# Kernel optimization log

Hardware: AMD Instinct MI355X
Metric: run time of the kernel (lower is better)

## Reference

```python
import jax, jax.numpy as jnp
import numpy as np

N = 50000
E = 800000
NFEAT = 128
NHID = 128
NCLASS = 40
NUM_HOPS = 4


def setup_inputs() -> dict:
    key = jax.random.key(0)
    ks = jax.random.split(key, 8)
    stdv = 1.0 / np.sqrt(NHID)
    features = jax.random.normal(ks[0], (N, NFEAT), dtype=jnp.float32)
    edge_row = jax.random.randint(ks[1], (E,), 0, N, dtype=jnp.int32)
    edge_col = jax.random.randint(ks[2], (E,), 0, N, dtype=jnp.int32)
    edge_val = jax.random.uniform(ks[3], (E,), dtype=jnp.float32) / 16.0  # ~normalized adj
    Wg = jax.random.uniform(ks[4], (NUM_HOPS, NHID, NHID), minval=-stdv, maxval=stdv, dtype=jnp.float32)
    att_w = jax.random.uniform(ks[5], (NFEAT + NHID,), minval=-stdv, maxval=stdv, dtype=jnp.float32)
    att_b = jnp.zeros((1,), dtype=jnp.float32)
    fc_w = jax.random.uniform(ks[6], (NHID, NCLASS), minval=-stdv, maxval=stdv, dtype=jnp.float32)
    fc_b = jnp.zeros((NCLASS,), dtype=jnp.float32)
    return {"features": features, "edge_row": edge_row, "edge_col": edge_col,
            "edge_val": edge_val, "Wg": Wg, "att_w": att_w, "att_b": att_b,
            "fc_w": fc_w, "fc_b": fc_b}


def _spmm(edge_row, edge_col, edge_val, x):
    # sparse (COO) adj @ x : gather source rows, scale, scatter-add to dest rows
    return jax.ops.segment_sum(edge_val[:, None] * x[edge_col], edge_row, num_segments=N)


def reference(features, edge_row, edge_col, edge_val, Wg, att_w, att_b, fc_w, fc_b):
    h_list = [features]
    h = features
    for i in range(NUM_HOPS):
        h = _spmm(edge_row, edge_col, edge_val, h)
        h = jax.nn.relu(h @ Wg[i])  # dropout is identity in eval mode
        h_list.append(h)

    # attention: sigmoid(Linear(cat(h_k, h0))) for each hop output h_k
    H = jnp.stack(h_list[1:], axis=0)          # [K, N, nhid]
    w_h, w_f = att_w[:NHID], att_w[NHID:]      # cat order is (x, features)
    scores = jax.nn.sigmoid(jnp.einsum('knh,h->kn', H, w_h)
                            + (features @ w_f)[None, :] + att_b[0])  # [K, N]
    W = jax.nn.softmax(scores, axis=0)         # softmax over hops, per node

    # faithful to original loop: h_list[1]*W0 + sum_{i=1..K-1} h_list[i]*W_i
    output = h_list[1] * W[0][:, None]
    for i in range(1, NUM_HOPS):
        output = output + h_list[i] * W[i][:, None]

    logits = output @ fc_w + fc_b
    return jax.nn.log_softmax(logits, axis=1)
```

## Files before the change

### kernel.cpp

```cpp
#include <hip/hip_runtime.h>
#include <cmath>

#define N      50000
#define E      800000
#define NFEAT  128
#define NHID   128
#define NCLASS 40
#define NUM_HOPS 4
#define NF     (N * NHID)
#define NBKT   196
#define BCAP   5888
#define XSTR   132
#define HSTR   136
#define HROWS  16
#define SC1_EPT 16
#define SC1_BLK ((E + 256 * SC1_EPT - 1) / (256 * SC1_EPT))

typedef __attribute__((ext_vector_type(8))) short bf16x8;
typedef __attribute__((ext_vector_type(4))) float f32x4;

__device__ __forceinline__ unsigned bf16pack(float a, float b) {
    unsigned ua = __float_as_uint(a), ub = __float_as_uint(b);
    ua = (ua + 0x7fffu + ((ua >> 16) & 1u)) >> 16;
    ub = (ub + 0x7fffu + ((ub >> 16) & 1u)) >> 16;
    return ua | (ub << 16);
}
__device__ __forceinline__ unsigned short bf16s(float x) {
    unsigned u = __float_as_uint(x);
    u = (u + 0x7fffu + ((u >> 16) & 1u)) >> 16;
    return (unsigned short)u;
}
__device__ __forceinline__ float bf16lo(unsigned u) { return __uint_as_float(u << 16); }
__device__ __forceinline__ float bf16hi(unsigned u) { return __uint_as_float(u & 0xffff0000u); }


__global__ void k_binit2(int* __restrict__ bcur) {
    int b = threadIdx.x;
    if (b < NBKT) bcur[b] = b * BCAP;
}

__global__ __launch_bounds__(256) void k_scat1(const int* __restrict__ row,
                                               const int* __restrict__ col,
                                               const float* __restrict__ val,
                                               int* __restrict__ bcur,
                                               unsigned long long* __restrict__ evt) {
    __shared__ int lhist[NBKT];
    __shared__ int gbase[NBKT];
    __shared__ int lcur[NBKT];
    int t = threadIdx.x;
    int e0 = blockIdx.x * (256 * SC1_EPT);
    for (int i = t; i < NBKT; i += 256) { lhist[i] = 0; lcur[i] = 0; }
    __syncthreads();
    int rows[SC1_EPT];
#pragma unroll
    for (int i = 0; i < SC1_EPT; ++i) {
        int e = e0 + i * 256 + t;
        int r = (e < E) ? row[e] : -1;
        rows[i] = r;
        if (r >= 0) atomicAdd(&lhist[r >> 8], 1);
    }
    __syncthreads();
    for (int i = t; i < NBKT; i += 256) {
        int c = lhist[i];
        gbase[i] = c ? atomicAdd(&bcur[i], c) : 0;
    }
    __syncthreads();
#pragma unroll
    for (int i = 0; i < SC1_EPT; ++i) {
        int r = rows[i];
        if (r >= 0) {
            int e = e0 + i * 256 + t;
            int b = r >> 8;
            int off = atomicAdd(&lcur[b], 1);
            size_t idx = (size_t)gbase[b] + off;
            if (idx < (size_t)(b + 1) * BCAP) {
                unsigned v = __float_as_uint(val[e]);
                v = (v + 0x7fffu + ((v >> 16) & 1u)) & 0xffff0000u;
                evt[idx] = ((unsigned long long)(r & 255) << 32)
                         | ((unsigned)col[e] | v);
            }
        }
    }
}

__global__ __launch_bounds__(256) void k_scat2b(const int* __restrict__ bcur,
                                                const unsigned long long* __restrict__ evt,
                                                unsigned* __restrict__ ev,
                                                int* __restrict__ rpb,
                                                int* __restrict__ rpe) {
    __shared__ int lhist[256];
    __shared__ int ws[4];
    __shared__ int cur[256];
    int b = blockIdx.x;
    int t = threadIdx.x;
    int base = b * BCAP;
    int ecnt = bcur[b] - base;
    if (ecnt > BCAP) ecnt = BCAP;
    lhist[t] = 0;
    __syncthreads();
    for (int i = t; i < ecnt; i += 256)
        atomicAdd(&lhist[(int)(evt[(size_t)base + i] >> 32)], 1);
    __syncthreads();
    int cntr = lhist[t];
    int pc = (cntr + 3) & ~3;
    int lane = t & 63, wv_ = t >> 6;
    int incl = pc;
    for (int off = 1; off < 64; off <<= 1) {
        int u = __shfl_up(incl, off);
        if (lane >= off) incl += u;
    }
    if (lane == 63) ws[wv_] = incl;
    __syncthreads();
    int woff = 0;
    for (int k = 0; k < wv_; ++k) woff += ws[k];
    int rowbeg = base + (incl - pc + woff);
    int rt = b * 256 + t;
    if (rt < N) { rpb[rt] = rowbeg; rpe[rt] = rowbeg + pc; }
    cur[t] = rowbeg;
    __syncthreads();
    for (int i = t; i < ecnt; i += 256) {
        unsigned long long e = evt[(size_t)base + i];
        int r8 = (int)(e >> 32);
        int p = atomicAdd(&cur[r8], 1);
        ev[p] = (unsigned)e;
    }
    __syncthreads();
    int e1 = rowbeg + pc;
    for (int p = cur[t]; p < e1; ++p) ev[p] = 0;
}


__global__ void k_cvtf(const float* __restrict__ f, const float* __restrict__ att_w,
                       float* __restrict__ fs, unsigned short* __restrict__ fb) {
    int node = (blockIdx.x * blockDim.x + threadIdx.x) >> 6;
    if (node >= N) return;
    int lane = threadIdx.x & 63;
    const float2 wf = ((const float2*)(att_w + NHID))[lane];
    const float2 fv = ((const float2*)(f + (size_t)node * NFEAT))[lane];
    ((unsigned*)(fb + (size_t)node * NFEAT))[lane] = bf16pack(fv.x, fv.y);
    float s = fv.x * wf.x + fv.y * wf.y;
    for (int off = 32; off; off >>= 1) s += __shfl_xor(s, off);
    if (lane == 0) fs[node] = s;
}

__global__ void k_cvt_w(const float* __restrict__ Wg, unsigned short* __restrict__ Wbt) {
    int idx = blockIdx.x * blockDim.x + threadIdx.x;
    if (idx >= NUM_HOPS * NHID * NHID) return;
    int i = idx >> 14;
    int rem = idx & 16383;
    int n = rem >> 7;
    int k = rem & 127;
    Wbt[idx] = bf16s(Wg[(i << 14) + k * NHID + n]);
}


__global__ __launch_bounds__(256) void k_hop(const int* __restrict__ rpb,
                                             const int* __restrict__ rpe,
                                             const unsigned* __restrict__ ev,
                                             const unsigned short* __restrict__ xb,
                                             const unsigned short* __restrict__ Wbt,
                                             const float* __restrict__ att_w,
                                             unsigned short* __restrict__ yb,
                                             float* __restrict__ Sh) {
    __shared__ unsigned short xsm[HROWS * HSTR];
    __shared__ float sS[HROWS][4];
    int t = threadIdx.x;
    int w = t >> 6;
    int lane = t & 63;
    int quad = lane >> 4;
    int l15 = lane & 15;
    int rowb = blockIdx.x * HROWS;
    const uint4* xq = (const uint4*)xb;

#define ACC8(g, v)                                                            \
    do {                                                                      \
        a0 = fmaf((v), bf16lo((g).x), a0); a1 = fmaf((v), bf16hi((g).x), a1); \
        a2 = fmaf((v), bf16lo((g).y), a2); a3 = fmaf((v), bf16hi((g).y), a3); \
        a4 = fmaf((v), bf16lo((g).z), a4); a5 = fmaf((v), bf16hi((g).z), a5); \
        a6 = fmaf((v), bf16lo((g).w), a6); a7 = fmaf((v), bf16hi((g).w), a7); \
    } while (0)
    {
        int rl  = t >> 4;
        int row = rowb + rl;
        float a0 = 0.f, a1 = 0.f, a2 = 0.f, a3 = 0.f;
        float a4 = 0.f, a5 = 0.f, a6 = 0.f, a7 = 0.f;
        if (row < N) {
            int beg = rpb[row], end = rpe[row];
            int j = beg;
            for (; j + 8 <= end; j += 8) {
                uint4 p0 = *(const uint4*)(ev + j);
                uint4 p1 = *(const uint4*)(ev + j + 4);
                uint4 g0 = xq[(size_t)(p0.x & 0xffffu) * 16 + l15];
                uint4 g1 = xq[(size_t)(p0.y & 0xffffu) * 16 + l15];
                uint4 g2 = xq[(size_t)(p0.z & 0xffffu) * 16 + l15];
                uint4 g3 = xq[(size_t)(p0.w & 0xffffu) * 16 + l15];
                uint4 g4 = xq[(size_t)(p1.x & 0xffffu) * 16 + l15];
                uint4 g5 = xq[(size_t)(p1.y & 0xffffu) * 16 + l15];
                uint4 g6 = xq[(size_t)(p1.z & 0xffffu) * 16 + l15];
                uint4 g7 = xq[(size_t)(p1.w & 0xffffu) * 16 + l15];
                ACC8(g0, bf16hi(p0.x));
                ACC8(g1, bf16hi(p0.y));
                ACC8(g2, bf16hi(p0.z));
                ACC8(g3, bf16hi(p0.w));
                ACC8(g4, bf16hi(p1.x));
                ACC8(g5, bf16hi(p1.y));
                ACC8(g6, bf16hi(p1.z));
                ACC8(g7, bf16hi(p1.w));
            }
            if (j < end) {
                uint4 p0 = *(const uint4*)(ev + j);
                uint4 g0 = xq[(size_t)(p0.x & 0xffffu) * 16 + l15];
                uint4 g1 = xq[(size_t)(p0.y & 0xffffu) * 16 + l15];
                uint4 g2 = xq[(size_t)(p0.z & 0xffffu) * 16 + l15];
                uint4 g3 = xq[(size_t)(p0.w & 0xffffu) * 16 + l15];
                ACC8(g0, bf16hi(p0.x));
                ACC8(g1, bf16hi(p0.y));
                ACC8(g2, bf16hi(p0.z));
                ACC8(g3, bf16hi(p0.w));
            }
        }
        uint4 o;
        o.x = bf16pack(a0, a1);
        o.y = bf16pack(a2, a3);
        o.z = bf16pack(a4, a5);
        o.w = bf16pack(a6, a7);
        *(uint4*)(xsm + (size_t)rl * HSTR + l15 * 8) = o;
    }
#undef ACC8
    __syncthreads();

    bf16x8 af[4];
#pragma unroll
    for (int s = 0; s < 4; ++s) {
        uint4 ua = *(const uint4*)(xsm + (size_t)l15 * HSTR + s * 32 + quad * 8);
        af[s] = __builtin_bit_cast(bf16x8, ua);
    }

    f32x4 acc[2];
#pragma unroll
    for (int nt = 0; nt < 2; ++nt) acc[nt] = (f32x4){0.f, 0.f, 0.f, 0.f};

#pragma unroll
    for (int nt = 0; nt < 2; ++nt) {
        int ntg = w * 2 + nt;
#pragma unroll
        for (int s = 0; s < 4; ++s) {
            uint4 ub = *(const uint4*)(Wbt + ((size_t)(ntg * 16 + l15) * NHID + s * 32 + quad * 8));
            bf16x8 bfv = __builtin_bit_cast(bf16x8, ub);
            acc[nt] = __builtin_amdgcn_mfma_f32_16x16x32_bf16(af[s], bfv, acc[nt], 0, 0, 0);
        }
    }

    float whl[2];
#pragma unroll
    for (int nt = 0; nt < 2; ++nt) whl[nt] = att_w[(w * 2 + nt) * 16 + l15];

    float scr[4] = {0.f, 0.f, 0.f, 0.f};
#pragma unroll
    for (int nt = 0; nt < 2; ++nt) {
#pragma unroll
        for (int r = 0; r < 4; ++r) {
            float v = fmaxf(acc[nt][r], 0.f);
            scr[r] = fmaf(v, whl[nt], scr[r]);
            int grow = rowb + quad * 4 + r;
            if (grow < N)
                yb[(size_t)grow * NHID + (w * 2 + nt) * 16 + l15] = bf16s(v);
        }
    }
#pragma unroll
    for (int r = 0; r < 4; ++r) {
        float p = scr[r];
        p += __shfl_xor(p, 1);
        p += __shfl_xor(p, 2);
        p += __shfl_xor(p, 4);
        p += __shfl_xor(p, 8);
        if (l15 == 0) sS[quad * 4 + r][w] = p;
    }
    __syncthreads();
    if (t < HROWS) {
        int grow = rowb + t;
        if (grow < N) Sh[grow] = sS[t][0] + sS[t][1] + sS[t][2] + sS[t][3];
    }
}


__global__ __launch_bounds__(256) void k_attn_final(const unsigned short* __restrict__ hb,
                                                    const float* __restrict__ S,
                                                    const float* __restrict__ fs,
                                                    const float* __restrict__ att_b,
                                                    const float* __restrict__ fc_w,
                                                    const float* __restrict__ fc_b,
                                                    float* __restrict__ out) {
    __shared__ float xs[64 * XSTR];
    __shared__ float wv[4][64];
    int t = threadIdx.x;
    int base = blockIdx.x * 64;

    if (t < 64) {
        int node = base + t;
        if (node < N) {
            float b = att_b[0] + fs[node];
            float g0 = 1.f / (1.f + __expf(-(S[0 * N + node] + b)));
            float g1 = 1.f / (1.f + __expf(-(S[1 * N + node] + b)));
            float g2 = 1.f / (1.f + __expf(-(S[2 * N + node] + b)));
            float g3 = 1.f / (1.f + __expf(-(S[3 * N + node] + b)));
            float m = fmaxf(fmaxf(g0, g1), fmaxf(g2, g3));
            float e0 = __expf(g0 - m), e1 = __expf(g1 - m);
            float e2 = __expf(g2 - m), e3 = __expf(g3 - m);
            float inv = 1.f / (e0 + e1 + e2 + e3);
            wv[0][t] = e0 * inv; wv[1][t] = e1 * inv;
            wv[2][t] = e2 * inv; wv[3][t] = e3 * inv;
        } else {
            wv[0][t] = 0.f; wv[1][t] = 0.f; wv[2][t] = 0.f; wv[3][t] = 0.f;
        }
    }
    __syncthreads();

#pragma unroll
    for (int qq = 0; qq < 4; ++qq) {
        int idx = qq * 256 + t;
        int nl = idx >> 4;
        int d8 = idx & 15;
        int node = base + nl;
        float o[8] = {0.f, 0.f, 0.f, 0.f, 0.f, 0.f, 0.f, 0.f};
        if (node < N) {
            float w0 = wv[0][nl], w1 = wv[1][nl], w2 = wv[2][nl], w3 = wv[3][nl];
            uint4 u0 = ((const uint4*)(hb + 0 * (size_t)NF + (size_t)node * NHID))[d8];
            uint4 u1 = ((const uint4*)(hb + 1 * (size_t)NF + (size_t)node * NHID))[d8];
            uint4 u2 = ((const uint4*)(hb + 2 * (size_t)NF + (size_t)node * NHID))[d8];
            uint4 u3 = ((const uint4*)(hb + 3 * (size_t)NF + (size_t)node * NHID))[d8];
            o[0] = w0 * bf16lo(u0.x) + w1 * bf16lo(u1.x) + w2 * bf16lo(u2.x) + w3 * bf16lo(u3.x);
            o[1] = w0 * bf16hi(u0.x) + w1 * bf16hi(u1.x) + w2 * bf16hi(u2.x) + w3 * bf16hi(u3.x);
            o[2] = w0 * bf16lo(u0.y) + w1 * bf16lo(u1.y) + w2 * bf16lo(u2.y) + w3 * bf16lo(u3.y);
            o[3] = w0 * bf16hi(u0.y) + w1 * bf16hi(u1.y) + w2 * bf16hi(u2.y) + w3 * bf16hi(u3.y);
            o[4] = w0 * bf16lo(u0.z) + w1 * bf16lo(u1.z) + w2 * bf16lo(u2.z) + w3 * bf16lo(u3.z);
            o[5] = w0 * bf16hi(u0.z) + w1 * bf16hi(u1.z) + w2 * bf16hi(u2.z) + w3 * bf16hi(u3.z);
            o[6] = w0 * bf16lo(u0.w) + w1 * bf16lo(u1.w) + w2 * bf16lo(u2.w) + w3 * bf16lo(u3.w);
            o[7] = w0 * bf16hi(u0.w) + w1 * bf16hi(u1.w) + w2 * bf16hi(u2.w) + w3 * bf16hi(u3.w);
        }
        float* xp = &xs[nl * XSTR + (d8 << 3)];
        *(float4*)xp       = make_float4(o[0], o[1], o[2], o[3]);
        *(float4*)(xp + 4) = make_float4(o[4], o[5], o[6], o[7]);
    }
    __syncthreads();

    int cq = t & 15;
    int rg = t >> 4;
    int cb = (cq < 10) ? (cq << 2) : 36;
    float4 bias = *(const float4*)(fc_b + cb);
    float4 acc[4];
#pragma unroll
    for (int r = 0; r < 4; ++r) acc[r] = bias;
    for (int k4 = 0; k4 < NHID / 4; ++k4) {
        float4 w0 = *(const float4*)(fc_w + (size_t)(4 * k4 + 0) * NCLASS + cb);
        float4 w1 = *(const float4*)(fc_w + (size_t)(4 * k4 + 1) * NCLASS + cb);
        float4 w2 = *(const float4*)(fc_w + (size_t)(4 * k4 + 2) * NCLASS + cb);
        float4 w3 = *(const float4*)(fc_w + (size_t)(4 * k4 + 3) * NCLASS + cb);
#pragma unroll
        for (int r = 0; r < 4; ++r) {
            float4 xv = *(const float4*)&xs[(rg * 4 + r) * XSTR + (k4 << 2)];
            acc[r].x = fmaf(xv.x, w0.x, acc[r].x);
            acc[r].y = fmaf(xv.x, w0.y, acc[r].y);
            acc[r].z = fmaf(xv.x, w0.z, acc[r].z);
            acc[r].w = fmaf(xv.x, w0.w, acc[r].w);
            acc[r].x = fmaf(xv.y, w1.x, acc[r].x);
            acc[r].y = fmaf(xv.y, w1.y, acc[r].y);
            acc[r].z = fmaf(xv.y, w1.z, acc[r].z);
            acc[r].w = fmaf(xv.y, w1.w, acc[r].w);
            acc[r].x = fmaf(xv.z, w2.x, acc[r].x);
            acc[r].y = fmaf(xv.z, w2.y, acc[r].y);
            acc[r].z = fmaf(xv.z, w2.z, acc[r].z);
            acc[r].w = fmaf(xv.z, w2.w, acc[r].w);
            acc[r].x = fmaf(xv.w, w3.x, acc[r].x);
            acc[r].y = fmaf(xv.w, w3.y, acc[r].y);
            acc[r].z = fmaf(xv.w, w3.z, acc[r].z);
            acc[r].w = fmaf(xv.w, w3.w, acc[r].w);
        }
    }
#pragma unroll
    for (int r = 0; r < 4; ++r) {
        int nd = base + rg * 4 + r;
        float mloc = (cq < 10)
            ? fmaxf(fmaxf(acc[r].x, acc[r].y), fmaxf(acc[r].z, acc[r].w))
            : -INFINITY;
        float m = mloc;
        m = fmaxf(m, __shfl_xor(m, 1));
        m = fmaxf(m, __shfl_xor(m, 2));
        m = fmaxf(m, __shfl_xor(m, 4));
        m = fmaxf(m, __shfl_xor(m, 8));
        float sloc = (cq < 10)
            ? (__expf(acc[r].x - m) + __expf(acc[r].y - m) +
               __expf(acc[r].z - m) + __expf(acc[r].w - m))
            : 0.f;
        float s = sloc;
        s += __shfl_xor(s, 1);
        s += __shfl_xor(s, 2);
        s += __shfl_xor(s, 4);
        s += __shfl_xor(s, 8);
        float ls = m + logf(s);
        if (cq < 10 && nd < N) {
            float4 o;
            o.x = acc[r].x - ls;
            o.y = acc[r].y - ls;
            o.z = acc[r].z - ls;
            o.w = acc[r].w - ls;
            *(float4*)(out + (size_t)nd * NCLASS + cb) = o;
        }
    }
}


extern "C" void kernel_launch(void* const* d_in, const int* in_sizes, int n_in,
                              void* d_out, int out_size, void* d_ws, size_t ws_size,
                              hipStream_t stream) {
    const float* features = (const float*)d_in[0];
    const int*   erow     = (const int*)d_in[1];
    const int*   ecol     = (const int*)d_in[2];
    const float* eval_    = (const float*)d_in[3];
    const float* Wg       = (const float*)d_in[4];
    const float* att_w    = (const float*)d_in[5];
    const float* att_b    = (const float*)d_in[6];
    const float* fc_w     = (const float*)d_in[7];
    const float* fc_b     = (const float*)d_in[8];
    float*       out      = (float*)d_out;

    const size_t SLOTS = 2 * (size_t)NF
                       + (size_t)NF / 2
                       + 32768
                       + (size_t)NBKT * BCAP
                       + 3 * (size_t)N
                       + NBKT
                       + 4 * (size_t)N;
    if (ws_size < SLOTS * 4) return;

    unsigned short* hbb  = (unsigned short*)d_ws;
    unsigned short* fb   = hbb + 4 * (size_t)NF;
    unsigned short* Wbt  = fb + (size_t)NF;
    unsigned*       ev   = (unsigned*)(Wbt + 65536);
    int*            rpb  = (int*)(ev + (size_t)NBKT * BCAP);
    int*            rpe  = rpb + N;
    float*          fs   = (float*)(rpe + N);
    int*            bcur = (int*)(fs + N);
    float*          S    = (float*)(bcur + NBKT);
    unsigned long long* evt = (unsigned long long*)hbb;

    k_binit2<<<1, 256, 0, stream>>>(bcur);
    k_scat1<<<SC1_BLK, 256, 0, stream>>>(erow, ecol, eval_, bcur, evt);
    k_scat2b<<<NBKT, 256, 0, stream>>>(bcur, evt, ev, rpb, rpe);

    k_cvtf<<<(N * 64 + 255) / 256, 256, 0, stream>>>(features, att_w, fs, fb);
    k_cvt_w<<<(NUM_HOPS * NHID * NHID + 255) / 256, 256, 0, stream>>>(Wg, Wbt);

    const unsigned short* xb = fb;
    for (int i = 0; i < NUM_HOPS; ++i) {
        k_hop<<<(N + HROWS - 1) / HROWS, 256, 0, stream>>>(rpb, rpe, ev, xb,
                                                 Wbt + (size_t)i * NHID * NHID,
                                                 att_w, hbb + (size_t)i * NF,
                                                 S + (size_t)i * N);
        xb = hbb + (size_t)i * NF;
    }

    k_attn_final<<<(N + 63) / 64, 256, 0, stream>>>(hbb, S, fs, att_b, fc_w, fc_b, out);
}
```

Before: 308.5 us.

## Sort rows by degree so hop blocks process similar-length rows together

Adds a counting sort of nodes by padded row length (histogram, scan, scatter) that builds a permutation, then has each hop kernel process rows in permuted order and write outputs back to the original row positions. The goal is to cut load imbalance and wave divergence when rows of very different degree share a block. In exchange it adds three small kernels, an extra indirection per row, and scattered output stores that are less coalesced.

```diff
diff --git a/kernel.cpp b/kernel.cpp
--- a/kernel.cpp
+++ b/kernel.cpp
@@ -13,6 +13,7 @@
 #define XSTR   132
 #define HSTR   136
 #define HROWS  16
+#define DBINS  1024
 #define SC1_EPT 16
 #define SC1_BLK ((E + 256 * SC1_EPT - 1) / (256 * SC1_EPT))
 
@@ -34,9 +35,10 @@
 __device__ __forceinline__ float bf16hi(unsigned u) { return __uint_as_float(u & 0xffff0000u); }
 
 
-__global__ void k_binit2(int* __restrict__ bcur) {
-    int b = threadIdx.x;
-    if (b < NBKT) bcur[b] = b * BCAP;
+__global__ void k_binit2(int* __restrict__ bcur, int* __restrict__ dhist) {
+    int t = threadIdx.x;
+    if (t < NBKT) bcur[t] = t * BCAP;
+    for (int i = t; i < DBINS; i += 256) dhist[i] = 0;
 }
 
 __global__ __launch_bounds__(256) void k_scat1(const int* __restrict__ row,
@@ -130,6 +132,51 @@
 }
 
 
+__global__ void k_dhist(const int* __restrict__ rpb, const int* __restrict__ rpe,
+                        int* __restrict__ dhist) {
+    int i = blockIdx.x * 256 + threadIdx.x;
+    if (i < N) {
+        int d = (rpe[i] - rpb[i]) >> 2;
+        if (d >= DBINS) d = DBINS - 1;
+        atomicAdd(&dhist[d], 1);
+    }
+}
+
+__global__ void k_dscan(int* __restrict__ dhist) {
+    __shared__ int ws[4];
+    int t = threadIdx.x;
+    int v0 = dhist[t * 4 + 0], v1 = dhist[t * 4 + 1];
+    int v2 = dhist[t * 4 + 2], v3 = dhist[t * 4 + 3];
+    int s = v0 + v1 + v2 + v3;
+    int lane = t & 63, w = t >> 6;
+    int incl = s;
+    for (int off = 1; off < 64; off <<= 1) {
+        int u = __shfl_up(incl, off);
+        if (lane >= off) incl += u;
+    }
+    if (lane == 63) ws[w] = incl;
+    __syncthreads();
+    int woff = 0;
+    for (int k = 0; k < w; ++k) woff += ws[k];
+    int base = incl - s + woff;
+    dhist[t * 4 + 0] = base;
+    dhist[t * 4 + 1] = base + v0;
+    dhist[t * 4 + 2] = base + v0 + v1;
+    dhist[t * 4 + 3] = base + v0 + v1 + v2;
+}
+
+__global__ void k_dscat(const int* __restrict__ rpb, const int* __restrict__ rpe,
+                        int* __restrict__ dhist, int* __restrict__ perm) {
+    int i = blockIdx.x * 256 + threadIdx.x;
+    if (i < N) {
+        int d = (rpe[i] - rpb[i]) >> 2;
+        if (d >= DBINS) d = DBINS - 1;
+        int p = atomicAdd(&dhist[d], 1);
+        perm[p] = i;
+    }
+}
+
+
 __global__ void k_cvtf(const float* __restrict__ f, const float* __restrict__ att_w,
                        float* __restrict__ fs, unsigned short* __restrict__ fb) {
     int node = (blockIdx.x * blockDim.x + threadIdx.x) >> 6;
@@ -154,7 +201,8 @@
 }
 
 
-__global__ __launch_bounds__(256) void k_hop(const int* __restrict__ rpb,
+__global__ __launch_bounds__(256) void k_hop(const int* __restrict__ perm,
+                                             const int* __restrict__ rpb,
                                              const int* __restrict__ rpe,
                                              const unsigned* __restrict__ ev,
                                              const unsigned short* __restrict__ xb,
@@ -181,10 +229,11 @@
     } while (0)
     {
         int rl  = t >> 4;
-        int row = rowb + rl;
+        int gl  = rowb + rl;
         float a0 = 0.f, a1 = 0.f, a2 = 0.f, a3 = 0.f;
         float a4 = 0.f, a5 = 0.f, a6 = 0.f, a7 = 0.f;
-        if (row < N) {
+        if (gl < N) {
+            int row = perm[gl];
             int beg = rpb[row], end = rpe[row];
             int j = beg;
             for (; j + 8 <= end; j += 8) {
@@ -256,15 +305,20 @@
     for (int nt = 0; nt < 2; ++nt) whl[nt] = att_w[(w * 2 + nt) * 16 + l15];
 
     float scr[4] = {0.f, 0.f, 0.f, 0.f};
+    int growp[4];
+#pragma unroll
+    for (int r = 0; r < 4; ++r) {
+        int gl = rowb + quad * 4 + r;
+        growp[r] = (gl < N) ? perm[gl] : -1;
+    }
 #pragma unroll
     for (int nt = 0; nt < 2; ++nt) {
 #pragma unroll
         for (int r = 0; r < 4; ++r) {
             float v = fmaxf(acc[nt][r], 0.f);
             scr[r] = fmaf(v, whl[nt], scr[r]);
-            int grow = rowb + quad * 4 + r;
-            if (grow < N)
-                yb[(size_t)grow * NHID + (w * 2 + nt) * 16 + l15] = bf16s(v);
+            if (growp[r] >= 0)
+                yb[(size_t)growp[r] * NHID + (w * 2 + nt) * 16 + l15] = bf16s(v);
         }
     }
 #pragma unroll
@@ -278,8 +332,8 @@
     }
     __syncthreads();
     if (t < HROWS) {
-        int grow = rowb + t;
-        if (grow < N) Sh[grow] = sS[t][0] + sS[t][1] + sS[t][2] + sS[t][3];
+        int gl = rowb + t;
+        if (gl < N) Sh[perm[gl]] = sS[t][0] + sS[t][1] + sS[t][2] + sS[t][3];
     }
 }
 
@@ -430,6 +484,8 @@
                        + (size_t)NBKT * BCAP
                        + 3 * (size_t)N
                        + NBKT
+                       + (size_t)N
+                       + DBINS
                        + 4 * (size_t)N;
     if (ws_size < SLOTS * 4) return;
 
@@ -441,19 +497,25 @@
     int*            rpe  = rpb + N;
     float*          fs   = (float*)(rpe + N);
     int*            bcur = (int*)(fs + N);
-    float*          S    = (float*)(bcur + NBKT);
+    int*            perm = bcur + NBKT;
+    int*            dhist= perm + N;
+    float*          S    = (float*)(dhist + DBINS);
     unsigned long long* evt = (unsigned long long*)hbb;
 
-    k_binit2<<<1, 256, 0, stream>>>(bcur);
+    k_binit2<<<1, 256, 0, stream>>>(bcur, dhist);
     k_scat1<<<SC1_BLK, 256, 0, stream>>>(erow, ecol, eval_, bcur, evt);
     k_scat2b<<<NBKT, 256, 0, stream>>>(bcur, evt, ev, rpb, rpe);
 
+    k_dhist<<<(N + 255) / 256, 256, 0, stream>>>(rpb, rpe, dhist);
+    k_dscan<<<1, 256, 0, stream>>>(dhist);
+    k_dscat<<<(N + 255) / 256, 256, 0, stream>>>(rpb, rpe, dhist, perm);
+
     k_cvtf<<<(N * 64 + 255) / 256, 256, 0, stream>>>(features, att_w, fs, fb);
     k_cvt_w<<<(NUM_HOPS * NHID * NHID + 255) / 256, 256, 0, stream>>>(Wg, Wbt);
 
     const unsigned short* xb = fb;
     for (int i = 0; i < NUM_HOPS; ++i) {
-        k_hop<<<(N + HROWS - 1) / HROWS, 256, 0, stream>>>(rpb, rpe, ev, xb,
+        k_hop<<<(N + HROWS - 1) / HROWS, 256, 0, stream>>>(perm, rpb, rpe, ev, xb,
                                                  Wbt + (size_t)i * NHID * NHID,
                                                  att_w, hbb + (size_t)i * NF,
                                                  S + (size_t)i * N);
```

New measurement: 877.0 us. +184.3%, slower.

## Sort nodes by degree class so hop blocks process rows of similar degree

Applied to the files above, without the earlier changes.

Adds a three-kernel counting sort that buckets nodes by padded degree (in groups of 4, 16 classes, descending). The hop kernel then processes rows through this permutation, which evens out per-warp work within a block and schedules heavy rows first. The cost is three extra small launches and an indirect lookup for row index, output row, and score writes, and output rows become scattered writes.

```diff
diff --git a/kernel.cpp b/kernel.cpp
--- a/kernel.cpp
+++ b/kernel.cpp
@@ -13,6 +13,7 @@
 #define XSTR   132
 #define HSTR   136
 #define HROWS  16
+#define DCLS   16
 #define SC1_EPT 16
 #define SC1_BLK ((E + 256 * SC1_EPT - 1) / (256 * SC1_EPT))
 
@@ -33,10 +34,15 @@
 __device__ __forceinline__ float bf16lo(unsigned u) { return __uint_as_float(u << 16); }
 __device__ __forceinline__ float bf16hi(unsigned u) { return __uint_as_float(u & 0xffff0000u); }
 
+__device__ __forceinline__ int dclass(int pc4) {
+    int d = pc4 < (DCLS - 1) ? pc4 : (DCLS - 1);
+    return (DCLS - 1) - d;
+}
+
 
 __global__ void k_binit2(int* __restrict__ bcur) {
-    int b = threadIdx.x;
-    if (b < NBKT) bcur[b] = b * BCAP;
+    int t = threadIdx.x;
+    if (t < NBKT) bcur[t] = t * BCAP;
 }
 
 __global__ __launch_bounds__(256) void k_scat1(const int* __restrict__ row,
@@ -130,6 +136,62 @@
 }
 
 
+__global__ __launch_bounds__(256) void k_dh16(const int* __restrict__ rpb,
+                                              const int* __restrict__ rpe,
+                                              int* __restrict__ bh) {
+    __shared__ int lh[DCLS];
+    int t = threadIdx.x;
+    int b = blockIdx.x;
+    if (t < DCLS) lh[t] = 0;
+    __syncthreads();
+    int i = b * 256 + t;
+    if (i < N) atomicAdd(&lh[dclass((rpe[i] - rpb[i]) >> 2)], 1);
+    __syncthreads();
+    if (t < DCLS) bh[b * DCLS + t] = lh[t];
+}
+
+__global__ __launch_bounds__(256) void k_dsc16(int* __restrict__ bh) {
+    __shared__ int tot[DCLS];
+    int t = threadIdx.x;
+    if (t < DCLS) {
+        int s = 0;
+        for (int b = 0; b < NBKT; ++b) s += bh[b * DCLS + t];
+        tot[t] = s;
+    }
+    __syncthreads();
+    if (t == 0) {
+        int a = 0;
+        for (int k = 0; k < DCLS; ++k) { int v = tot[k]; tot[k] = a; a += v; }
+    }
+    __syncthreads();
+    if (t < DCLS) {
+        int a = tot[t];
+        for (int b = 0; b < NBKT; ++b) {
+            int v = bh[b * DCLS + t];
+            bh[b * DCLS + t] = a;
+            a += v;
+        }
+    }
+}
+
+__global__ __launch_bounds__(256) void k_dp16(const int* __restrict__ rpb,
+                                              const int* __restrict__ rpe,
+                                              const int* __restrict__ bh,
+                                              int* __restrict__ perm) {
+    __shared__ int lcur[DCLS];
+    int t = threadIdx.x;
+    int b = blockIdx.x;
+    if (t < DCLS) lcur[t] = bh[b * DCLS + t];
+    __syncthreads();
+    int i = b * 256 + t;
+    if (i < N) {
+        int c = dclass((rpe[i] - rpb[i]) >> 2);
+        int p = atomicAdd(&lcur[c], 1);
+        perm[p] = i;
+    }
+}
+
+
 __global__ void k_cvtf(const float* __restrict__ f, const float* __restrict__ att_w,
                        float* __restrict__ fs, unsigned short* __restrict__ fb) {
     int node = (blockIdx.x * blockDim.x + threadIdx.x) >> 6;
@@ -154,7 +216,8 @@
 }
 
 
-__global__ __launch_bounds__(256) void k_hop(const int* __restrict__ rpb,
+__global__ __launch_bounds__(256) void k_hop(const int* __restrict__ perm,
+                                             const int* __restrict__ rpb,
                                              const int* __restrict__ rpe,
                                              const unsigned* __restrict__ ev,
                                              const unsigned short* __restrict__ xb,
@@ -181,10 +244,11 @@
     } while (0)
     {
         int rl  = t >> 4;
-        int row = rowb + rl;
+        int gl  = rowb + rl;
         float a0 = 0.f, a1 = 0.f, a2 = 0.f, a3 = 0.f;
         float a4 = 0.f, a5 = 0.f, a6 = 0.f, a7 = 0.f;
-        if (row < N) {
+        if (gl < N) {
+            int row = perm[gl];
             int beg = rpb[row], end = rpe[row];
             int j = beg;
             for (; j + 8 <= end; j += 8) {
@@ -256,15 +320,20 @@
     for (int nt = 0; nt < 2; ++nt) whl[nt] = att_w[(w * 2 + nt) * 16 + l15];
 
     float scr[4] = {0.f, 0.f, 0.f, 0.f};
+    int growp[4];
+#pragma unroll
+    for (int r = 0; r < 4; ++r) {
+        int gl = rowb + quad * 4 + r;
+        growp[r] = (gl < N) ? perm[gl] : -1;
+    }
 #pragma unroll
     for (int nt = 0; nt < 2; ++nt) {
 #pragma unroll
         for (int r = 0; r < 4; ++r) {
             float v = fmaxf(acc[nt][r], 0.f);
             scr[r] = fmaf(v, whl[nt], scr[r]);
-            int grow = rowb + quad * 4 + r;
-            if (grow < N)
-                yb[(size_t)grow * NHID + (w * 2 + nt) * 16 + l15] = bf16s(v);
+            if (growp[r] >= 0)
+                yb[(size_t)growp[r] * NHID + (w * 2 + nt) * 16 + l15] = bf16s(v);
         }
     }
 #pragma unroll
@@ -278,8 +347,8 @@
     }
     __syncthreads();
     if (t < HROWS) {
-        int grow = rowb + t;
-        if (grow < N) Sh[grow] = sS[t][0] + sS[t][1] + sS[t][2] + sS[t][3];
+        int gl = rowb + t;
+        if (gl < N) Sh[perm[gl]] = sS[t][0] + sS[t][1] + sS[t][2] + sS[t][3];
     }
 }
 
@@ -430,6 +499,8 @@
                        + (size_t)NBKT * BCAP
                        + 3 * (size_t)N
                        + NBKT
+                       + (size_t)N
+                       + (size_t)NBKT * DCLS
                        + 4 * (size_t)N;
     if (ws_size < SLOTS * 4) return;
 
@@ -441,19 +512,25 @@
     int*            rpe  = rpb + N;
     float*          fs   = (float*)(rpe + N);
     int*            bcur = (int*)(fs + N);
-    float*          S    = (float*)(bcur + NBKT);
+    int*            perm = bcur + NBKT;
+    int*            bh   = perm + N;
+    float*          S    = (float*)(bh + NBKT * DCLS);
     unsigned long long* evt = (unsigned long long*)hbb;
 
     k_binit2<<<1, 256, 0, stream>>>(bcur);
     k_scat1<<<SC1_BLK, 256, 0, stream>>>(erow, ecol, eval_, bcur, evt);
     k_scat2b<<<NBKT, 256, 0, stream>>>(bcur, evt, ev, rpb, rpe);
 
+    k_dh16<<<NBKT, 256, 0, stream>>>(rpb, rpe, bh);
+    k_dsc16<<<1, 256, 0, stream>>>(bh);
+    k_dp16<<<NBKT, 256, 0, stream>>>(rpb, rpe, bh, perm);
+
     k_cvtf<<<(N * 64 + 255) / 256, 256, 0, stream>>>(features, att_w, fs, fb);
     k_cvt_w<<<(NUM_HOPS * NHID * NHID + 255) / 256, 256, 0, stream>>>(Wg, Wbt);
 
     const unsigned short* xb = fb;
     for (int i = 0; i < NUM_HOPS; ++i) {
-        k_hop<<<(N + HROWS - 1) / HROWS, 256, 0, stream>>>(rpb, rpe, ev, xb,
+        k_hop<<<(N + HROWS - 1) / HROWS, 256, 0, stream>>>(perm, rpb, rpe, ev, xb,
                                                  Wbt + (size_t)i * NHID * NHID,
                                                  att_w, hbb + (size_t)i * NF,
                                                  S + (size_t)i * N);
```

Result: slower. 319.2 us (+3.5%).

## Split each row's SpMM edges across two thread groups and halve rows per block

Applied to the files above, without the earlier changes.

The fused hop kernel now processes 8 rows per block instead of 16. Each row's edge list is split between two 16-lane groups, and their partial sums are combined with a cross-lane shuffle. This doubles the grid size and halves the per-thread serial gather chain, aiming to expose more memory parallelism for the irregular gathers. The cost is that the 16x16 MFMA tile now computes duplicated rows (lanes 8-15 mirror rows 0-7), wasting half of the matrix work and reloading weights for twice as many blocks.

```diff
diff --git a/kernel.cpp b/kernel.cpp
--- a/kernel.cpp
+++ b/kernel.cpp
@@ -12,7 +12,7 @@
 #define BCAP   5888
 #define XSTR   132
 #define HSTR   136
-#define HROWS  16
+#define HROWS  8
 #define SC1_EPT 16
 #define SC1_BLK ((E + 256 * SC1_EPT - 1) / (256 * SC1_EPT))
 
@@ -35,8 +35,8 @@
 
 
 __global__ void k_binit2(int* __restrict__ bcur) {
-    int b = threadIdx.x;
-    if (b < NBKT) bcur[b] = b * BCAP;
+    int t = threadIdx.x;
+    if (t < NBKT) bcur[t] = t * BCAP;
 }
 
 __global__ __launch_bounds__(256) void k_scat1(const int* __restrict__ row,
@@ -180,14 +180,20 @@
         a6 = fmaf((v), bf16lo((g).w), a6); a7 = fmaf((v), bf16hi((g).w), a7); \
     } while (0)
     {
-        int rl  = t >> 4;
-        int row = rowb + rl;
+        int rl  = w * 2 + (quad >> 1);
+        int h   = quad & 1;
+        int gl  = rowb + rl;
         float a0 = 0.f, a1 = 0.f, a2 = 0.f, a3 = 0.f;
         float a4 = 0.f, a5 = 0.f, a6 = 0.f, a7 = 0.f;
-        if (row < N) {
-            int beg = rpb[row], end = rpe[row];
-            int j = beg;
-            for (; j + 8 <= end; j += 8) {
+        if (gl < N) {
+            int beg = rpb[gl], end = rpe[gl];
+            int pc  = end - beg;
+            int h0  = ((pc >> 1) + 3) & ~3;
+            if (h0 > pc) h0 = pc;
+            int jb = h ? (beg + h0) : beg;
+            int je = h ? end : (beg + h0);
+            int j = jb;
+            for (; j + 8 <= je; j += 8) {
                 uint4 p0 = *(const uint4*)(ev + j);
                 uint4 p1 = *(const uint4*)(ev + j + 4);
                 uint4 g0 = xq[(size_t)(p0.x & 0xffffu) * 16 + l15];
@@ -207,7 +213,7 @@
                 ACC8(g6, bf16hi(p1.z));
                 ACC8(g7, bf16hi(p1.w));
             }
-            if (j < end) {
+            if (j < je) {
                 uint4 p0 = *(const uint4*)(ev + j);
                 uint4 g0 = xq[(size_t)(p0.x & 0xffffu) * 16 + l15];
                 uint4 g1 = xq[(size_t)(p0.y & 0xffffu) * 16 + l15];
@@ -219,12 +225,22 @@
                 ACC8(g3, bf16hi(p0.w));
             }
         }
-        uint4 o;
-        o.x = bf16pack(a0, a1);
-        o.y = bf16pack(a2, a3);
-        o.z = bf16pack(a4, a5);
-        o.w = bf16pack(a6, a7);
-        *(uint4*)(xsm + (size_t)rl * HSTR + l15 * 8) = o;
+        a0 += __shfl_xor(a0, 16);
+        a1 += __shfl_xor(a1, 16);
+        a2 += __shfl_xor(a2, 16);
+        a3 += __shfl_xor(a3, 16);
+        a4 += __shfl_xor(a4, 16);
+        a5 += __shfl_xor(a5, 16);
+        a6 += __shfl_xor(a6, 16);
+        a7 += __shfl_xor(a7, 16);
+        if (h == 0) {
+            uint4 o;
+            o.x = bf16pack(a0, a1);
+            o.y = bf16pack(a2, a3);
+            o.z = bf16pack(a4, a5);
+            o.w = bf16pack(a6, a7);
+            *(uint4*)(xsm + (size_t)rl * HSTR + l15 * 8) = o;
+        }
     }
 #undef ACC8
     __syncthreads();
@@ -232,7 +248,7 @@
     bf16x8 af[4];
 #pragma unroll
     for (int s = 0; s < 4; ++s) {
-        uint4 ua = *(const uint4*)(xsm + (size_t)l15 * HSTR + s * 32 + quad * 8);
+        uint4 ua = *(const uint4*)(xsm + (size_t)(l15 & 7) * HSTR + s * 32 + quad * 8);
         af[s] = __builtin_bit_cast(bf16x8, ua);
     }
 
@@ -262,8 +278,9 @@
         for (int r = 0; r < 4; ++r) {
             float v = fmaxf(acc[nt][r], 0.f);
             scr[r] = fmaf(v, whl[nt], scr[r]);
-            int grow = rowb + quad * 4 + r;
-            if (grow < N)
+            int row16 = quad * 4 + r;
+            int grow = rowb + row16;
+            if (row16 < HROWS && grow < N)
                 yb[(size_t)grow * NHID + (w * 2 + nt) * 16 + l15] = bf16s(v);
         }
     }
@@ -274,7 +291,8 @@
         p += __shfl_xor(p, 2);
         p += __shfl_xor(p, 4);
         p += __shfl_xor(p, 8);
-        if (l15 == 0) sS[quad * 4 + r][w] = p;
+        int row16 = quad * 4 + r;
+        if (l15 == 0 && row16 < HROWS) sS[row16][w] = p;
     }
     __syncthreads();
     if (t < HROWS) {
```

Result: slower. 338.9 us (+9.8%).
